# Performance work log

Hardware: AMD Instinct MI355X
Metric: run time of the kernel (lower is better)

The kernel has to match this reference:

```python
import jax, jax.numpy as jnp
import numpy as np

N_NODES, N_EDGES, N_RELS, D_IN, D_OUT = 50000, 200000, 64, 32, 32


def setup_inputs() -> dict:
    key = jax.random.key(0)
    k1, k2, k3, k4, k5 = jax.random.split(key, 5)
    feat = jax.random.normal(k1, (N_NODES, D_IN), dtype=jnp.float32)
    # learned per-relation projection weights: [R, D_IN, D_OUT]
    weight = jax.random.normal(k2, (N_RELS, D_IN, D_OUT), dtype=jnp.float32) * 0.05
    src = jax.random.randint(k3, (N_EDGES,), 0, N_NODES)
    dst = jax.random.randint(k4, (N_EDGES,), 0, N_NODES)
    etypes = jax.random.randint(k5, (N_EDGES,), 0, N_RELS)
    return {"feat": feat, "weight": weight, "src": src, "dst": dst, "etypes": etypes}


def reference(feat, weight, src, dst, etypes):
    # gather source features and per-edge relation weights (HighMem variant
    # materializes W[etypes] just like torch index_select), then per-edge bmm
    n_nodes = feat.shape[0]
    msg = jnp.einsum('ei,eio->eo', feat[src], weight[etypes])  # [E, D_OUT]
    out = jax.ops.segment_sum(msg, dst, num_segments=n_nodes)  # [N, D_OUT]
    return out
```

## Files before the change

kernel.cpp:

```cpp
#include <hip/hip_runtime.h>


#define D 32
#define NRELS 64
#define BLOCK 1024
#define WPB (BLOCK / 64)
#define GRID 256
#define MAXCHUNK 1024
#define MAXTILES (NRELS + MAXCHUNK / 16)

typedef __bf16 bf16x8 __attribute__((ext_vector_type(8)));
typedef float  f32x4  __attribute__((ext_vector_type(4)));

static __device__ __forceinline__ unsigned int f2b(float x) {
    unsigned int u = __float_as_uint(x);
    return (u + 0x7fffu + ((u >> 16) & 1u)) >> 16;
}


__global__ __launch_bounds__(256) void prep_kernel(
    const float* __restrict__ feat, const float* __restrict__ weight,
    unsigned short* __restrict__ featb,
    unsigned short* __restrict__ wpack,
    int n_nodes)
{
    int idx = blockIdx.x * 256 + threadIdx.x;
    int nfeat = n_nodes * 4;
    if (idx < nfeat) {
        const float4* fp = (const float4*)(feat + (size_t)idx * 8);
        float4 a = fp[0], b = fp[1];
        uint4 o;
        o.x = f2b(a.x) | (f2b(a.y) << 16);
        o.y = f2b(a.z) | (f2b(a.w) << 16);
        o.z = f2b(b.x) | (f2b(b.y) << 16);
        o.w = f2b(b.z) | (f2b(b.w) << 16);
        ((uint4*)featb)[idx] = o;
    } else if (idx < nfeat + NRELS * 2 * 64) {
        int t = idx - nfeat;
        int r = t >> 7, half = (t >> 6) & 1, lane = t & 63;
        int quad = lane >> 4, n = lane & 15;
        const float* W = weight + (size_t)r * (D * D) + half * 16 + n;
        uint4 o;
        unsigned int v[8];
        #pragma unroll
        for (int j = 0; j < 8; ++j) v[j] = f2b(W[(quad * 8 + j) * D]);
        o.x = v[0] | (v[1] << 16);
        o.y = v[2] | (v[3] << 16);
        o.z = v[4] | (v[5] << 16);
        o.w = v[6] | (v[7] << 16);
        ((uint4*)wpack)[t] = o;
    }
}


__global__ __launch_bounds__(BLOCK, 4) void rgcn_fused_kernel(
    const unsigned short* __restrict__ featb,
    const unsigned short* __restrict__ wpack,
    const int* __restrict__ src,
    const int* __restrict__ dst,
    const int* __restrict__ etypes,
    float* __restrict__ out,
    int E, int chunk)
{
    __shared__ int cnt[NRELS];
    __shared__ int off[NRELS];
    __shared__ unsigned short list[MAXCHUNK];
    __shared__ unsigned short desc[MAXTILES];
    __shared__ int ntile_sh;

    int tid = threadIdx.x;
    int gbase = blockIdx.x * chunk;

    if (tid < NRELS) cnt[tid] = 0;
    __syncthreads();

    int my_r = -1, my_rank = 0;
    if (tid < chunk && gbase + tid < E) {
        my_r = etypes[gbase + tid];
        my_rank = atomicAdd(&cnt[my_r], 1);
    }
    __syncthreads();

    if (tid < 64) {
        int c = cnt[tid];
        int x = c;
        #pragma unroll
        for (int o = 1; o < 64; o <<= 1) {
            int y = __shfl_up(x, o, 64);
            if (tid >= o) x += y;
        }
        off[tid] = x - c;

        int nt = (c + 15) >> 4;
        int tx = nt;
        #pragma unroll
        for (int o = 1; o < 64; o <<= 1) {
            int y = __shfl_up(tx, o, 64);
            if (tid >= o) tx += y;
        }
        int tbase = tx - nt;
        for (int t = 0; t < nt; ++t)
            desc[tbase + t] = (unsigned short)((tid << 8) | t);
        if (tid == 63) ntile_sh = tx;
    }
    __syncthreads();

    if (my_r >= 0) list[off[my_r] + my_rank] = (unsigned short)tid;
    int ntiles = ntile_sh;
    __syncthreads();

    int wave = tid >> 6;
    int lane = tid & 63;
    int n    = lane & 15;
    int quad = lane >> 4;

    int per = (ntiles + WPB - 1) / WPB;
    int t0 = wave * per;
    int t1 = t0 + per; if (t1 > ntiles) t1 = ntiles;

    for (int ti = t0; ti < t1; ++ti) {
        int dsc = desc[ti];
        int r = dsc >> 8;
        int t = dsc & 255;
        int c = cnt[r];
        int mbase = t * 16;
        int mcnt = c - mbase; if (mcnt > 16) mcnt = 16;
        int lbase = off[r] + mbase;

        bf16x8 b0 = *(const bf16x8*)(wpack + ((size_t)(r * 2 + 0) * 64 + lane) * 8);
        bf16x8 b1 = *(const bf16x8*)(wpack + ((size_t)(r * 2 + 1) * 64 + lane) * 8);

        int mm = (n < mcnt) ? n : 0;
        int le = list[lbase + mm];
        int s  = src[gbase + le];
        bf16x8 a = *(const bf16x8*)(featb + (size_t)s * D + quad * 8);

        f32x4 z = {0.f, 0.f, 0.f, 0.f};
        f32x4 c0 = __builtin_amdgcn_mfma_f32_16x16x32_bf16(a, b0, z, 0, 0, 0);
        f32x4 c1 = __builtin_amdgcn_mfma_f32_16x16x32_bf16(a, b1, z, 0, 0, 0);

        #pragma unroll
        for (int v = 0; v < 4; ++v) {
            int m2 = quad * 4 + v;
            if (m2 < mcnt) {
                int le2 = list[lbase + m2];
                int d = dst[gbase + le2];
                atomicAdd(out + (size_t)d * D + n,      c0[v]);
                atomicAdd(out + (size_t)d * D + 16 + n, c1[v]);
            }
        }
    }
}


__global__ __launch_bounds__(256) void rgcn_edge_kernel(
    const float* __restrict__ feat, const float* __restrict__ weight,
    const int* __restrict__ src, const int* __restrict__ dst,
    const int* __restrict__ etypes, float* __restrict__ out, int n_edges)
{
    int gid = blockIdx.x * blockDim.x + threadIdx.x;
    int e = gid >> 5;
    int o = gid & 31;
    if (e >= n_edges) return;
    int s = src[e], d = dst[e], r = etypes[e];
    const float* W = weight + (size_t)r * (D * D);
    float fv = feat[(size_t)s * D + o];
    float acc = 0.f;
    #pragma unroll
    for (int i = 0; i < D; ++i) {
        float fi = __shfl(fv, i, 32);
        acc = fmaf(fi, W[i * D + o], acc);
    }
    atomicAdd(&out[(size_t)d * D + o], acc);
}


extern "C" void kernel_launch(void* const* d_in, const int* in_sizes, int n_in,
                              void* d_out, int out_size, void* d_ws, size_t ws_size,
                              hipStream_t stream) {
    const float* feat   = (const float*)d_in[0];
    const float* weight = (const float*)d_in[1];
    const int*   src    = (const int*)d_in[2];
    const int*   dst    = (const int*)d_in[3];
    const int*   etypes = (const int*)d_in[4];
    float*       out    = (float*)d_out;

    int N = in_sizes[0] / D;
    int R = in_sizes[1] / (D * D);
    int E = in_sizes[2];

    hipMemsetAsync(d_out, 0, (size_t)out_size * sizeof(float), stream);

    int chunk = (E + GRID - 1) / GRID;
    size_t featb_elems = (size_t)N * D;
    size_t need = (featb_elems + (size_t)NRELS * 2 * 64 * 8) * sizeof(unsigned short);

    if (R != NRELS || chunk > MAXCHUNK || ws_size < need) {
        long long total = (long long)E * 32;
        int grid = (int)((total + 255) / 256);
        rgcn_edge_kernel<<<grid, 256, 0, stream>>>(feat, weight, src, dst,
                                                   etypes, out, E);
        return;
    }

    unsigned short* featb = (unsigned short*)d_ws;
    unsigned short* wpack = featb + featb_elems;

    int prep_tasks = N * 4 + NRELS * 2 * 64;
    int prep_grid = (prep_tasks + 255) / 256;
    prep_kernel<<<prep_grid, 256, 0, stream>>>(feat, weight, featb, wpack, N);

    rgcn_fused_kernel<<<GRID, BLOCK, 0, stream>>>(featb, wpack, src, dst,
                                                  etypes, out, E, chunk);
}
```

Measured before the change: 94.99 us.

## Replace global atomic scatter with bucketed counting-sort and shared-memory reduction

Edges are bucketed by destination node (64 nodes per bucket) using a histogram in the prep kernel, a single-block scan and atomic cursors. The message kernel then writes each per-edge message to its bucket slot instead of doing global float atomics. A new gather kernel reduces each bucket in shared memory and writes the output directly, which also removes the output memset. The cost is a per-edge message buffer that must be written and read back (about 25 MB), two extra kernel launches and global atomics on the cursors.

New measurement: 275.2 us. 2.9x slower.

```diff
diff --git a/kernel.cpp b/kernel.cpp
--- a/kernel.cpp
+++ b/kernel.cpp
@@ -8,6 +8,7 @@
 #define GRID 256
 #define MAXCHUNK 1024
 #define MAXTILES (NRELS + MAXCHUNK / 16)
+#define BUCKET 64
 
 typedef __bf16 bf16x8 __attribute__((ext_vector_type(8)));
 typedef float  f32x4  __attribute__((ext_vector_type(4)));
@@ -20,9 +21,11 @@
 
 __global__ __launch_bounds__(256) void prep_kernel(
     const float* __restrict__ feat, const float* __restrict__ weight,
+    const int* __restrict__ dst,
     unsigned short* __restrict__ featb,
     unsigned short* __restrict__ wpack,
-    int n_nodes)
+    int* __restrict__ hist,
+    int n_nodes, int E)
 {
     int idx = blockIdx.x * 256 + threadIdx.x;
     int nfeat = n_nodes * 4;
@@ -50,16 +53,51 @@
         o.w = v[6] | (v[7] << 16);
         ((uint4*)wpack)[t] = o;
     }
-}
-
-
-__global__ __launch_bounds__(BLOCK, 4) void rgcn_fused_kernel(
+    if (idx < E) atomicAdd(&hist[dst[idx] >> 6], 1);
+}
+
+
+__global__ __launch_bounds__(1024) void scan_kernel(
+    const int* __restrict__ hist, int* __restrict__ base, int nb)
+{
+    __shared__ int wsum[16];
+    int tid = threadIdx.x;
+    int lane = tid & 63, wave = tid >> 6;
+    int v = (tid < nb) ? hist[tid] : 0;
+    int x = v;
+    #pragma unroll
+    for (int o = 1; o < 64; o <<= 1) {
+        int y = __shfl_up(x, o, 64);
+        if (lane >= o) x += y;
+    }
+    if (lane == 63) wsum[wave] = x;
+    __syncthreads();
+    if (wave == 0) {
+        int s = (lane < 16) ? wsum[lane] : 0;
+        #pragma unroll
+        for (int o = 1; o < 16; o <<= 1) {
+            int y = __shfl_up(s, o, 64);
+            if (lane >= o) s += y;
+        }
+        if (lane < 16) wsum[lane] = s;
+    }
+    __syncthreads();
+    int woff = (wave > 0) ? wsum[wave - 1] : 0;
+    int excl = x + woff - v;
+    if (tid <= nb) base[tid] = excl;
+}
+
+
+__global__ __launch_bounds__(BLOCK, 4) void msg_kernel(
     const unsigned short* __restrict__ featb,
     const unsigned short* __restrict__ wpack,
     const int* __restrict__ src,
     const int* __restrict__ dst,
     const int* __restrict__ etypes,
-    float* __restrict__ out,
+    const int* __restrict__ base,
+    int* __restrict__ cursor,
+    float* __restrict__ msg,
+    unsigned char* __restrict__ dloc,
     int E, int chunk)
 {
     __shared__ int cnt[NRELS];
@@ -67,6 +105,7 @@
     __shared__ unsigned short list[MAXCHUNK];
     __shared__ unsigned short desc[MAXTILES];
     __shared__ int ntile_sh;
+    __shared__ int pos_sh[MAXCHUNK];
 
     int tid = threadIdx.x;
     int gbase = blockIdx.x * chunk;
@@ -76,8 +115,14 @@
 
     int my_r = -1, my_rank = 0;
     if (tid < chunk && gbase + tid < E) {
-        my_r = etypes[gbase + tid];
+        int e = gbase + tid;
+        my_r = etypes[e];
         my_rank = atomicAdd(&cnt[my_r], 1);
+        int d = dst[e];
+        int b = d >> 6;
+        int p = base[b] + atomicAdd(&cursor[b], 1);
+        pos_sh[tid] = p;
+        dloc[p] = (unsigned char)(d & (BUCKET - 1));
     }
     __syncthreads();
 
@@ -143,13 +188,40 @@
         for (int v = 0; v < 4; ++v) {
             int m2 = quad * 4 + v;
             if (m2 < mcnt) {
-                int le2 = list[lbase + m2];
-                int d = dst[gbase + le2];
-                atomicAdd(out + (size_t)d * D + n,      c0[v]);
-                atomicAdd(out + (size_t)d * D + 16 + n, c1[v]);
+                int p2 = pos_sh[list[lbase + m2]];
+                msg[(size_t)p2 * D + n]      = c0[v];
+                msg[(size_t)p2 * D + 16 + n] = c1[v];
             }
         }
     }
+}
+
+
+__global__ __launch_bounds__(512) void gather_kernel(
+    const float* __restrict__ msg,
+    const unsigned char* __restrict__ dloc,
+    const int* __restrict__ base,
+    float* __restrict__ out, int n_nodes)
+{
+    __shared__ float acc[BUCKET * D];
+    int b = blockIdx.x;
+    int tid = threadIdx.x;
+    for (int j = tid; j < BUCKET * D; j += 512) acc[j] = 0.f;
+    __syncthreads();
+
+    int e0 = base[b], e1 = base[b + 1];
+    int g = tid >> 5, o = tid & 31;
+    for (int i = e0 + g; i < e1; i += 16) {
+        float m = msg[(size_t)i * D + o];
+        int dl = dloc[i];
+        atomicAdd(&acc[dl * D + o], m);
+    }
+    __syncthreads();
+
+    int node0 = b * BUCKET;
+    int nn = n_nodes - node0; if (nn > BUCKET) nn = BUCKET;
+    for (int j = tid; j < nn * D; j += 512)
+        out[(size_t)node0 * D + j] = acc[j];
 }
 
 
@@ -188,14 +260,27 @@
     int N = in_sizes[0] / D;
     int R = in_sizes[1] / (D * D);
     int E = in_sizes[2];
-
-    hipMemsetAsync(d_out, 0, (size_t)out_size * sizeof(float), stream);
-
+    int NB = (N + BUCKET - 1) / BUCKET;
     int chunk = (E + GRID - 1) / GRID;
-    size_t featb_elems = (size_t)N * D;
-    size_t need = (featb_elems + (size_t)NRELS * 2 * 64 * 8) * sizeof(unsigned short);
-
-    if (R != NRELS || chunk > MAXCHUNK || ws_size < need) {
+
+    size_t featb_off = 0;
+    size_t featb_sz  = ((size_t)N * D * 2 + 15) & ~(size_t)15;
+    size_t wpack_off = featb_off + featb_sz;
+    size_t wpack_sz  = (size_t)NRELS * 2 * 64 * 8 * 2;
+    size_t msg_off   = wpack_off + wpack_sz;
+    size_t msg_sz    = (size_t)E * D * 4;
+    size_t dloc_off  = msg_off + msg_sz;
+    size_t dloc_sz   = ((size_t)E + 15) & ~(size_t)15;
+    size_t hist_off  = dloc_off + dloc_sz;
+    size_t hist_sz   = (size_t)NB * 4;
+    size_t curs_off  = hist_off + hist_sz;
+    size_t curs_sz   = (size_t)NB * 4;
+    size_t base_off  = curs_off + curs_sz;
+    size_t base_sz   = (size_t)(NB + 1) * 4;
+    size_t need      = base_off + base_sz;
+
+    if (R != NRELS || chunk > MAXCHUNK || NB + 1 > 1024 || ws_size < need) {
+        hipMemsetAsync(d_out, 0, (size_t)out_size * sizeof(float), stream);
         long long total = (long long)E * 32;
         int grid = (int)((total + 255) / 256);
         rgcn_edge_kernel<<<grid, 256, 0, stream>>>(feat, weight, src, dst,
@@ -203,13 +288,27 @@
         return;
     }
 
-    unsigned short* featb = (unsigned short*)d_ws;
-    unsigned short* wpack = featb + featb_elems;
-
-    int prep_tasks = N * 4 + NRELS * 2 * 64;
-    int prep_grid = (prep_tasks + 255) / 256;
-    prep_kernel<<<prep_grid, 256, 0, stream>>>(feat, weight, featb, wpack, N);
-
-    rgcn_fused_kernel<<<GRID, BLOCK, 0, stream>>>(featb, wpack, src, dst,
-                                                  etypes, out, E, chunk);
-}
+    char* ws = (char*)d_ws;
+    unsigned short* featb = (unsigned short*)(ws + featb_off);
+    unsigned short* wpack = (unsigned short*)(ws + wpack_off);
+    float*          msg   = (float*)(ws + msg_off);
+    unsigned char*  dloc  = (unsigned char*)(ws + dloc_off);
+    int*            hist  = (int*)(ws + hist_off);
+    int*            curs  = (int*)(ws + curs_off);
+    int*            basep = (int*)(ws + base_off);
+
+    hipMemsetAsync(hist, 0, hist_sz + curs_sz, stream);
+
+    int nfeat = N * 4;
+    int prep_tasks = nfeat + NRELS * 2 * 64;
+    if (prep_tasks < E) prep_tasks = E;
+    prep_kernel<<<(prep_tasks + 255) / 256, 256, 0, stream>>>(
+        feat, weight, dst, featb, wpack, hist, N, E);
+
+    scan_kernel<<<1, 1024, 0, stream>>>(hist, basep, NB);
+
+    msg_kernel<<<GRID, BLOCK, 0, stream>>>(featb, wpack, src, dst, etypes,
+                                           basep, curs, msg, dloc, E, chunk);
+
+    gather_kernel<<<NB, 512, 0, stream>>>(msg, dloc, basep, out, N);
+}
```

## Partition output by destination slices and accumulate in shared memory

Applied to the files above, without the earlier changes.

Replaces global float atomics on the output with per-block destination slices: a prep pass packs dst/SLICE bytes, each block scans all edges to collect those hitting its slice, buckets them by relation, runs the bf16 MFMA tiles and accumulates into LDS before a plain coalesced store. This removes the output memset and the global atomic traffic. In exchange, every block redundantly scans the whole packed dst array, and edges beyond a fixed per-slice capacity would be silently dropped for skewed inputs.

Result: slower. 139.6 us (+47.0%).

```diff
diff --git a/kernel.cpp b/kernel.cpp
--- a/kernel.cpp
+++ b/kernel.cpp
@@ -4,10 +4,11 @@
 #define D 32
 #define NRELS 64
 #define BLOCK 1024
-#define WPB (BLOCK / 64)
-#define GRID 256
-#define MAXCHUNK 1024
-#define MAXTILES (NRELS + MAXCHUNK / 16)
+#define NSLICE 256
+#define SLICE 196
+#define ASTRIDE 33
+#define CAP 1536
+#define MAXDESC (NRELS + CAP / 16)
 
 typedef __bf16 bf16x8 __attribute__((ext_vector_type(8)));
 typedef float  f32x4  __attribute__((ext_vector_type(4)));
@@ -20,12 +21,15 @@
 
 __global__ __launch_bounds__(256) void prep_kernel(
     const float* __restrict__ feat, const float* __restrict__ weight,
+    const int* __restrict__ dst,
     unsigned short* __restrict__ featb,
     unsigned short* __restrict__ wpack,
-    int n_nodes)
+    unsigned int*  __restrict__ dstb4,
+    int n_nodes, int E)
 {
     int idx = blockIdx.x * 256 + threadIdx.x;
     int nfeat = n_nodes * 4;
+    int nwp = NRELS * 2 * 64;
     if (idx < nfeat) {
         const float4* fp = (const float4*)(feat + (size_t)idx * 8);
         float4 a = fp[0], b = fp[1];
@@ -35,51 +39,87 @@
         o.z = f2b(b.x) | (f2b(b.y) << 16);
         o.w = f2b(b.z) | (f2b(b.w) << 16);
         ((uint4*)featb)[idx] = o;
-    } else if (idx < nfeat + NRELS * 2 * 64) {
+    } else if (idx < nfeat + nwp) {
         int t = idx - nfeat;
         int r = t >> 7, half = (t >> 6) & 1, lane = t & 63;
         int quad = lane >> 4, n = lane & 15;
         const float* W = weight + (size_t)r * (D * D) + half * 16 + n;
+        unsigned int v[8];
+        #pragma unroll
+        for (int j = 0; j < 8; ++j) v[j] = f2b(W[(quad * 8 + j) * D]);
         uint4 o;
-        unsigned int v[8];
-        #pragma unroll
-        for (int j = 0; j < 8; ++j) v[j] = f2b(W[(quad * 8 + j) * D]);
         o.x = v[0] | (v[1] << 16);
         o.y = v[2] | (v[3] << 16);
         o.z = v[4] | (v[5] << 16);
         o.w = v[6] | (v[7] << 16);
         ((uint4*)wpack)[t] = o;
-    }
-}
-
-
-__global__ __launch_bounds__(BLOCK, 4) void rgcn_fused_kernel(
+    } else {
+        int j = idx - nfeat - nwp;
+        int nw = (E + 3) >> 2;
+        if (j < nw) {
+            unsigned int w = 0;
+            #pragma unroll
+            for (int k = 0; k < 4; ++k) {
+                int e = 4 * j + k;
+                if (e < E) w |= (unsigned int)(dst[e] / SLICE) << (8 * k);
+            }
+            dstb4[j] = w;
+        }
+    }
+}
+
+
+__global__ __launch_bounds__(BLOCK) void rgcn_slice_kernel(
     const unsigned short* __restrict__ featb,
     const unsigned short* __restrict__ wpack,
     const int* __restrict__ src,
     const int* __restrict__ dst,
     const int* __restrict__ etypes,
+    const unsigned int* __restrict__ dstb4,
     float* __restrict__ out,
-    int E, int chunk)
+    int N, int E)
 {
-    __shared__ int cnt[NRELS];
-    __shared__ int off[NRELS];
-    __shared__ unsigned short list[MAXCHUNK];
-    __shared__ unsigned short desc[MAXTILES];
-    __shared__ int ntile_sh;
+    __shared__ float acc[SLICE * ASTRIDE];
+    __shared__ unsigned int list[CAP];
+    __shared__ unsigned int list2[CAP];
+    __shared__ int srcl[CAP];
+    __shared__ unsigned short desc[MAXDESC];
+    __shared__ int cnt[NRELS], off[NRELS], cur[NRELS];
+    __shared__ int nmatch_sh, ntile_sh;
 
     int tid = threadIdx.x;
-    int gbase = blockIdx.x * chunk;
-
+    int b = blockIdx.x;
+    int lo = b * SLICE;
+
+    for (int j = tid; j < SLICE * ASTRIDE; j += BLOCK) acc[j] = 0.f;
     if (tid < NRELS) cnt[tid] = 0;
-    __syncthreads();
-
-    int my_r = -1, my_rank = 0;
-    if (tid < chunk && gbase + tid < E) {
-        my_r = etypes[gbase + tid];
-        my_rank = atomicAdd(&cnt[my_r], 1);
-    }
-    __syncthreads();
+    if (tid == 0) nmatch_sh = 0;
+    __syncthreads();
+
+    int nw = (E + 3) >> 2;
+    unsigned int target = (unsigned int)b;
+    for (int j = tid; j < nw; j += BLOCK) {
+        unsigned int w = dstb4[j];
+        #pragma unroll
+        for (int k = 0; k < 4; ++k) {
+            if (((w >> (8 * k)) & 255u) == target) {
+                int e = 4 * j + k;
+                if (e < E) {
+                    int loc = dst[e] - lo;
+                    int r = etypes[e];
+                    int idx = atomicAdd(&nmatch_sh, 1);
+                    if (idx < CAP) {
+                        list[idx] = ((unsigned int)e << 14) |
+                                    ((unsigned int)r << 8) | (unsigned int)loc;
+                        atomicAdd(&cnt[r], 1);
+                    }
+                }
+            }
+        }
+    }
+    __syncthreads();
+
+    int M = nmatch_sh; if (M > CAP) M = CAP;
 
     if (tid < 64) {
         int c = cnt[tid];
@@ -90,6 +130,7 @@
             if (tid >= o) x += y;
         }
         off[tid] = x - c;
+        cur[tid] = x - c;
 
         int nt = (c + 15) >> 4;
         int tx = nt;
@@ -105,20 +146,23 @@
     }
     __syncthreads();
 
-    if (my_r >= 0) list[off[my_r] + my_rank] = (unsigned short)tid;
+    for (int j = tid; j < M; j += BLOCK) {
+        unsigned int p = list[j];
+        int r = (p >> 8) & 63;
+        int slot = atomicAdd(&cur[r], 1);
+        list2[slot] = p;
+        srcl[slot] = src[p >> 14];
+    }
+    __syncthreads();
+
     int ntiles = ntile_sh;
-    __syncthreads();
 
     int wave = tid >> 6;
     int lane = tid & 63;
     int n    = lane & 15;
     int quad = lane >> 4;
 
-    int per = (ntiles + WPB - 1) / WPB;
-    int t0 = wave * per;
-    int t1 = t0 + per; if (t1 > ntiles) t1 = ntiles;
-
-    for (int ti = t0; ti < t1; ++ti) {
+    for (int ti = wave; ti < ntiles; ti += BLOCK / 64) {
         int dsc = desc[ti];
         int r = dsc >> 8;
         int t = dsc & 255;
@@ -131,8 +175,7 @@
         bf16x8 b1 = *(const bf16x8*)(wpack + ((size_t)(r * 2 + 1) * 64 + lane) * 8);
 
         int mm = (n < mcnt) ? n : 0;
-        int le = list[lbase + mm];
-        int s  = src[gbase + le];
+        int s  = srcl[lbase + mm];
         bf16x8 a = *(const bf16x8*)(featb + (size_t)s * D + quad * 8);
 
         f32x4 z = {0.f, 0.f, 0.f, 0.f};
@@ -143,13 +186,17 @@
         for (int v = 0; v < 4; ++v) {
             int m2 = quad * 4 + v;
             if (m2 < mcnt) {
-                int le2 = list[lbase + m2];
-                int d = dst[gbase + le2];
-                atomicAdd(out + (size_t)d * D + n,      c0[v]);
-                atomicAdd(out + (size_t)d * D + 16 + n, c1[v]);
+                int loc = (int)(list2[lbase + m2] & 255u);
+                atomicAdd(&acc[loc * ASTRIDE + n],      c0[v]);
+                atomicAdd(&acc[loc * ASTRIDE + 16 + n], c1[v]);
             }
         }
     }
+    __syncthreads();
+
+    int lim = N - lo; if (lim > SLICE) lim = SLICE;
+    for (int j = tid; j < lim * D; j += BLOCK)
+        out[(size_t)lo * D + j] = acc[(j >> 5) * ASTRIDE + (j & 31)];
 }
 
 
@@ -188,14 +235,21 @@
     int N = in_sizes[0] / D;
     int R = in_sizes[1] / (D * D);
     int E = in_sizes[2];
-
-    hipMemsetAsync(d_out, 0, (size_t)out_size * sizeof(float), stream);
-
-    int chunk = (E + GRID - 1) / GRID;
-    size_t featb_elems = (size_t)N * D;
-    size_t need = (featb_elems + (size_t)NRELS * 2 * 64 * 8) * sizeof(unsigned short);
-
-    if (R != NRELS || chunk > MAXCHUNK || ws_size < need) {
+    int nw = (E + 3) / 4;
+
+    size_t featb_off = 0;
+    size_t featb_sz  = ((size_t)N * D * 2 + 15) & ~(size_t)15;
+    size_t wpack_off = featb_off + featb_sz;
+    size_t wpack_sz  = (size_t)NRELS * 2 * 64 * 8 * 2;
+    size_t dstb_off  = wpack_off + wpack_sz;
+    size_t dstb_sz   = (size_t)nw * 4;
+    size_t need      = dstb_off + dstb_sz;
+
+    bool ok = (R == NRELS) && (N <= NSLICE * SLICE) && (E <= 220000)
+           && (ws_size >= need);
+
+    if (!ok) {
+        hipMemsetAsync(d_out, 0, (size_t)out_size * sizeof(float), stream);
         long long total = (long long)E * 32;
         int grid = (int)((total + 255) / 256);
         rgcn_edge_kernel<<<grid, 256, 0, stream>>>(feat, weight, src, dst,
@@ -203,13 +257,15 @@
         return;
     }
 
-    unsigned short* featb = (unsigned short*)d_ws;
-    unsigned short* wpack = featb + featb_elems;
-
-    int prep_tasks = N * 4 + NRELS * 2 * 64;
-    int prep_grid = (prep_tasks + 255) / 256;
-    prep_kernel<<<prep_grid, 256, 0, stream>>>(feat, weight, featb, wpack, N);
-
-    rgcn_fused_kernel<<<GRID, BLOCK, 0, stream>>>(featb, wpack, src, dst,
-                                                  etypes, out, E, chunk);
-}
+    char* ws = (char*)d_ws;
+    unsigned short* featb = (unsigned short*)(ws + featb_off);
+    unsigned short* wpack = (unsigned short*)(ws + wpack_off);
+    unsigned int*   dstb4 = (unsigned int*)(ws + dstb_off);
+
+    int prep_tasks = N * 4 + NRELS * 2 * 64 + nw;
+    prep_kernel<<<(prep_tasks + 255) / 256, 256, 0, stream>>>(
+        feat, weight, dst, featb, wpack, dstb4, N, E);
+
+    rgcn_slice_kernel<<<NSLICE, BLOCK, 0, stream>>>(
+        featb, wpack, src, dst, etypes, dstb4, out, N, E);
+}
```
